# Performance work log

Hardware: AMD Instinct MI355X
Metric: run time of the kernel (lower is better)

## Reference

```python
import jax, jax.numpy as jnp
import numpy as np

D = 1024       # d_model
DR = 1024      # d_rec
FFN = 4096     # ffn_inner
K = 4          # conv_kernel
B, T = 2, 4096
CHUNK = 64
EPS = 1e-6


def setup_inputs() -> dict:
    key = jax.random.key(0)
    ks = jax.random.split(key, 8)
    s = lambda k, shape, scale: jax.random.normal(k, shape, jnp.float32) * scale
    db = np.zeros((DR,), np.float32)
    q = DR // 4
    db[:q] = -2.2
    db[q:3 * q] = 0.0
    db[3 * q:] = 4.6
    return {
        "x": s(ks[0], (B, T, D), 1.0),
        "pre_norm_w": jnp.ones((D,), jnp.float32),
        "conv_w": s(ks[1], (D, 1, K), 0.3),
        "conv_b": jnp.zeros((D,), jnp.float32),
        "w_a": s(ks[2], (DR, D), 0.02),
        "w_i": s(ks[3], (DR, D), 0.02),
        "w_v": s(ks[4], (DR, D), 0.02),
        "out_proj_w": s(ks[5], (D, DR), 0.02),
        "decay_bias": jnp.asarray(db),
        "ffn_norm_w": jnp.ones((D,), jnp.float32),
        "w_gate_up": s(ks[6], (2 * FFN, D), 0.02),
        "w_down": s(ks[7], (D, FFN), 0.02),
    }


def rmsnorm(x, w):
    return x * jax.lax.rsqrt(jnp.mean(x * x, axis=-1, keepdims=True) + EPS) * w


def lin(x, w):  # nn.Linear weight layout (out, in)
    return jnp.einsum('btd,od->bto', x, w)


def causal_conv(h, w, b):
    # depthwise causal conv: h (B,T,D), w (D,1,K)
    hc = jnp.transpose(h, (0, 2, 1))  # (B,D,T)
    out = jax.lax.conv_general_dilated(
        hc, w, window_strides=(1,), padding=[(K - 1, 0)],
        dimension_numbers=('NCH', 'OIH', 'NCH'), feature_group_count=D)
    return jnp.transpose(out, (0, 2, 1)) + b


def chunked_scan(a, v):
    b, s, d = a.shape
    pad = (-s) % CHUNK
    af = jnp.pad(a, ((0, 0), (0, pad), (0, 0)), constant_values=1.0)
    vf = jnp.pad(v, ((0, 0), (0, pad), (0, 0)))
    n = (s + pad) // CHUNK
    dc = af.reshape(b, n, CHUNK, d)
    vc = vf.reshape(b, n, CHUNK, d)
    cum_decay = jnp.exp(jnp.cumsum(jnp.log(jnp.clip(dc, 1e-10)), axis=2))
    intra = cum_decay * jnp.cumsum(vc / jnp.clip(cum_decay, 1e-10), axis=2)

    def step(state, xs):
        cd, it = xs  # (B,CHUNK,d) each
        cs = it + cd * state[:, None, :]
        return cs[:, -1], cs

    _, states = jax.lax.scan(
        step, jnp.zeros((b, d), jnp.float32),
        (jnp.transpose(cum_decay, (1, 0, 2, 3)), jnp.transpose(intra, (1, 0, 2, 3))))
    return jnp.transpose(states, (1, 0, 2, 3)).reshape(b, n * CHUNK, d)[:, :s]


def reference(x, pre_norm_w, conv_w, conv_b, w_a, w_i, w_v, out_proj_w,
              decay_bias, ffn_norm_w, w_gate_up, w_down):
    h = rmsnorm(x, pre_norm_w)
    h = causal_conv(h, conv_w, conv_b)
    a = jax.nn.sigmoid(lin(h, w_a) + decay_bias)
    i_gate = jax.nn.sigmoid(lin(h, w_i))
    v = lin(h, w_v)
    input_signal = jnp.sqrt(jnp.clip(1.0 - a * a, 1e-8)) * (i_gate * v)
    rec_out = chunked_scan(a, input_signal).astype(x.dtype)
    x = x + lin(rec_out, out_proj_w)
    hn = rmsnorm(x, ffn_norm_w)
    gu = lin(hn, w_gate_up)
    gate, up = gu[..., :FFN], gu[..., FFN:]
    x = x + lin(jax.nn.silu(gate) * up, w_down)
    return x
```

## Files before the change

### kernel.cpp

```cpp
#include <hip/hip_runtime.h>

typedef __bf16 bf16_t;
typedef bf16_t bf16x4 __attribute__((ext_vector_type(4)));
typedef bf16_t bf16x8 __attribute__((ext_vector_type(8)));
typedef float f32x4 __attribute__((ext_vector_type(4)));

#define DD 1024
#define TT 4096

__device__ __forceinline__ void gload16(const void* g, void* l) {
    __builtin_amdgcn_global_load_lds(
        (const __attribute__((address_space(1))) void*)g,
        (__attribute__((address_space(3))) void*)l, 16, 0, 0);
}

__global__ __launch_bounds__(256) void cvt_bf16_k(const float* __restrict__ s,
                                                  bf16_t* __restrict__ d, int n) {
    int i = (blockIdx.x * 256 + threadIdx.x) * 4;
    if (i < n) {
        const float4 v = *(const float4*)(s + i);
        bf16x4 o;
        o[0] = (bf16_t)v.x; o[1] = (bf16_t)v.y; o[2] = (bf16_t)v.z; o[3] = (bf16_t)v.w;
        *(bf16x4*)(d + i) = o;
    }
}

__global__ __launch_bounds__(256) void cvt_ileave_k(const float* __restrict__ s0,
                                                    const float* __restrict__ s1,
                                                    bf16_t* __restrict__ d, int total) {
    int i = (blockIdx.x * 256 + threadIdx.x) * 4;
    if (i < total) {
        const int rp = i >> 10, k = i & 1023;
        const int c = rp >> 1;
        const float* src = ((rp & 1) ? s1 : s0) + (long)c * 1024 + k;
        const float4 v = *(const float4*)src;
        bf16x4 o;
        o[0] = (bf16_t)v.x; o[1] = (bf16_t)v.y; o[2] = (bf16_t)v.z; o[3] = (bf16_t)v.w;
        *(bf16x4*)(d + i) = o;
    }
}

__global__ __launch_bounds__(256) void rmsnorm_k(const float* __restrict__ x,
                                                 const float* __restrict__ w,
                                                 bf16_t* __restrict__ ob) {
    const long row = blockIdx.x;
    const float* xr = x + row * DD;
    const int t4 = threadIdx.x * 4;
    float4 v = *(const float4*)(xr + t4);
    float s = v.x*v.x + v.y*v.y + v.z*v.z + v.w*v.w;
    #pragma unroll
    for (int off = 1; off < 64; off <<= 1) s += __shfl_xor(s, off);
    __shared__ float red[4];
    if ((threadIdx.x & 63) == 0) red[threadIdx.x >> 6] = s;
    __syncthreads();
    float tot = red[0] + red[1] + red[2] + red[3];
    float sc = rsqrtf(tot * (1.0f / DD) + 1e-6f);
    float4 wv = *(const float4*)(w + t4);
    bf16x4 o;
    o[0] = (bf16_t)(v.x*sc*wv.x); o[1] = (bf16_t)(v.y*sc*wv.y);
    o[2] = (bf16_t)(v.z*sc*wv.z); o[3] = (bf16_t)(v.w*sc*wv.w);
    *(bf16x4*)(ob + row * DD + t4) = o;
}

__global__ __launch_bounds__(256) void conv_k(const bf16_t* __restrict__ h,
                                              const float* __restrict__ cw,
                                              const float* __restrict__ cb,
                                              bf16_t* __restrict__ hc) {
    const long idx = (long)blockIdx.x * 256 + threadIdx.x;
    const int d = (int)(idx & (DD - 1));
    const long bt = idx >> 10;
    const int t = (int)(bt & (TT - 1));
    const float w0 = cw[d*4+0], w1 = cw[d*4+1], w2 = cw[d*4+2], w3 = cw[d*4+3];
    const bf16_t* hp = h + bt * DD + d;
    float acc = cb[d] + (float)hp[0] * w3;
    if (t >= 1) acc += (float)hp[-DD]     * w2;
    if (t >= 2) acc += (float)hp[-2*DD]   * w1;
    if (t >= 3) acc += (float)hp[-3*DD]   * w0;
    hc[idx] = (bf16_t)acc;
}

__global__ __launch_bounds__(256) void scan1_k(const float* __restrict__ ap,
                                               const bf16_t* __restrict__ sp,
                                               float* __restrict__ cd63,
                                               float* __restrict__ i63) {
    const int d = blockIdx.x * 256 + threadIdx.x;
    const int c = blockIdx.y;
    const int b = blockIdx.z;
    const long rowbase = (long)b * TT + (long)c * 64;
    float la = 0.0f, rs = 0.0f, cdv = 0.0f, it = 0.0f;
    for (int t = 0; t < 64; t++) {
        const long off = (rowbase + t) * DD + d;
        const float a = ap[off];
        const float s = (float)sp[off];
        const float sig = sqrtf(fmaxf(1.0f - a * a, 1e-8f)) * s;
        la += __logf(fmaxf(a, 1e-10f));
        cdv = __expf(la);
        rs += sig / fmaxf(cdv, 1e-10f);
        it = cdv * rs;
    }
    const long o = ((long)b * 64 + c) * DD + d;
    cd63[o] = cdv;
    i63[o]  = it;
}

__global__ __launch_bounds__(256) void scan2_k(const float* __restrict__ cd63,
                                               const float* __restrict__ i63,
                                               float* __restrict__ carry_in) {
    const int g = blockIdx.x * 256 + threadIdx.x;
    const int b = g >> 10, d = g & (DD - 1);
    float st = 0.0f;
    for (int c = 0; c < 64; c++) {
        const long o = ((long)b * 64 + c) * DD + d;
        carry_in[o] = st;
        st = i63[o] + cd63[o] * st;
    }
}

__global__ __launch_bounds__(256) void scan3_k(const float* __restrict__ ap,
                                               const bf16_t* __restrict__ sp,
                                               const float* __restrict__ carry_in,
                                               bf16_t* __restrict__ rec) {
    const int d = blockIdx.x * 256 + threadIdx.x;
    const int c = blockIdx.y;
    const int b = blockIdx.z;
    const long rowbase = (long)b * TT + (long)c * 64;
    const float carry = carry_in[((long)b * 64 + c) * DD + d];
    float la = 0.0f, rs = 0.0f;
    for (int t = 0; t < 64; t++) {
        const long off = (rowbase + t) * DD + d;
        const float a = ap[off];
        const float s = (float)sp[off];
        const float sig = sqrtf(fmaxf(1.0f - a * a, 1e-8f)) * s;
        la += __logf(fmaxf(a, 1e-10f));
        const float cdv = __expf(la);
        rs += sig / fmaxf(cdv, 1e-10f);
        rec[off] = (bf16_t)(cdv * rs + cdv * carry);
    }
}

enum { EPI_AIV = 0, EPI_ADDRES = 1, EPI_GU = 3 };

template<int EPI, int NREP>
__global__ __launch_bounds__(512, 2) void gemm2p_k(const bf16_t* __restrict__ Ag,
                                                   const bf16_t* __restrict__ Bg,
                                                   int M, int N, int K,
                                                   float* outF, bf16_t* outB,
                                                   const float* aux, int ldc) {
    constexpr int BN  = NREP * 64;
    constexpr int ASZ = 16384;
    constexpr int BSZ = BN * 64;
    constexpr int BUF = ASZ + BSZ;
    extern __shared__ bf16_t smem[];
    const int tid = threadIdx.x;
    const int l = tid & 63;
    const int w = tid >> 6;
    const int wm = w >> 2, wn = w & 3;

    const int gx = gridDim.x;
    const int gy = gridDim.y;
    const int lin = blockIdx.y * gx + blockIdx.x;
    long row0, col0;
    if ((gy & 7) == 0) {
        const int rpc = gy >> 3;
        const int q = lin >> 3;
        row0 = (long)((lin & 7) * rpc + q % rpc) * 256;
        col0 = (long)(q / rpc) * (long)BN;
    } else {
        row0 = (long)blockIdx.y * 256;
        col0 = (long)blockIdx.x * BN;
    }

    const int srow = l >> 3;
    const int scol = ((l & 7) ^ srow) * 8;
    const long aBase = row0 + srow;
    const long bBase = col0 + srow;
    const int R0a = w * 32;
    const int R0b = w * (BN / 8);

    const int NT = K >> 6;
    f32x4 acc[8][NREP] = {};

    const int lq2 = (l >> 4) * 16;
    const int rA = wm * 128 + (l & 15);
    const int rB = wn * (NREP * 16) + (l & 15);
    const int eA0 = rA * 64 + ((lq2 ^ ((rA & 7) << 4)) >> 1);
    const int eB0 = ASZ + rB * 64 + ((lq2 ^ ((rB & 7) << 4)) >> 1);

    #define STAGE_A(tt, off)                                                          \
        { const long kgk = (long)(tt) * 64 + scol;                                    \
          _Pragma("unroll")                                                           \
          for (int i = 0; i < 4; i++)                                                 \
              gload16(Ag + (aBase + R0a + i * 8) * (long)K + kgk,                     \
                      &smem[(off) + (R0a + i * 8) * 64]); }
    #define STAGE_B(tt, off)                                                          \
        { const long kgk = (long)(tt) * 64 + scol;                                    \
          _Pragma("unroll")                                                           \
          for (int i = 0; i < NREP; i++)                                              \
              gload16(Bg + (bBase + R0b + i * 8) * (long)K + kgk,                     \
                      &smem[(off) + ASZ + (R0b + i * 8) * 64]); }

    STAGE_A(0, 0); STAGE_B(0, 0);
    STAGE_A(1, BUF); STAGE_B(1, BUF);
    if constexpr (NREP == 4) { asm volatile("s_waitcnt vmcnt(8)" ::: "memory"); }
    else                     { asm volatile("s_waitcnt vmcnt(6)" ::: "memory"); }
    asm volatile("s_barrier" ::: "memory");

    bf16x8 pA[2][4], pB[2][NREP];
    #pragma unroll
    for (int kk = 0; kk < 2; kk++) {
        const int xo = kk * 32;
        #pragma unroll
        for (int n = 0; n < NREP; n++)
            pB[kk][n] = *(const bf16x8*)&smem[(eB0 ^ xo) + n * 1024];
        #pragma unroll
        for (int m = 0; m < 4; m++)
            pA[kk][m] = *(const bf16x8*)&smem[(eA0 ^ xo) + m * 1024];
    }

    for (int t = 0; t < NT; t++) {
        const int co = (t & 1) ? BUF : 0;
        const int oo = BUF - co;
        bf16x8 a1[2][4];

        __builtin_amdgcn_s_setprio(1);
        #pragma unroll
        for (int kk = 0; kk < 2; kk++)
            #pragma unroll
            for (int m = 0; m < 4; m++)
                #pragma unroll
                for (int n = 0; n < NREP; n++)
                    acc[m][n] = __builtin_amdgcn_mfma_f32_16x16x32_bf16(pA[kk][m], pB[kk][n], acc[m][n], 0, 0, 0);
        __builtin_amdgcn_s_setprio(0);
        #pragma unroll
        for (int kk = 0; kk < 2; kk++) {
            const int xo = kk * 32;
            #pragma unroll
            for (int m = 0; m < 4; m++)
                a1[kk][m] = *(const bf16x8*)&smem[co + (eA0 ^ xo) + 4096 + m * 1024];
        }
        asm volatile("s_barrier" ::: "memory");

        if (t + 2 < NT) { STAGE_A(t + 2, co); STAGE_B(t + 2, co); }
        __builtin_amdgcn_s_setprio(1);
        #pragma unroll
        for (int kk = 0; kk < 2; kk++)
            #pragma unroll
            for (int m = 0; m < 4; m++)
                #pragma unroll
                for (int n = 0; n < NREP; n++)
                    acc[m + 4][n] = __builtin_amdgcn_mfma_f32_16x16x32_bf16(a1[kk][m], pB[kk][n], acc[m + 4][n], 0, 0, 0);
        __builtin_amdgcn_s_setprio(0);
        if (t + 2 < NT) {
            if constexpr (NREP == 4) { asm volatile("s_waitcnt vmcnt(8)" ::: "memory"); }
            else                     { asm volatile("s_waitcnt vmcnt(6)" ::: "memory"); }
        } else if (t + 1 < NT) {
            asm volatile("s_waitcnt vmcnt(0)" ::: "memory");
        }
        asm volatile("s_barrier" ::: "memory");
        if (t + 1 < NT) {
            #pragma unroll
            for (int kk = 0; kk < 2; kk++) {
                const int xo = kk * 32;
                #pragma unroll
                for (int n = 0; n < NREP; n++)
                    pB[kk][n] = *(const bf16x8*)&smem[oo + (eB0 ^ xo) + n * 1024];
                #pragma unroll
                for (int m = 0; m < 4; m++)
                    pA[kk][m] = *(const bf16x8*)&smem[oo + (eA0 ^ xo) + m * 1024];
            }
        }
    }
    #undef STAGE_A
    #undef STAGE_B

    #pragma unroll
    for (int m = 0; m < 8; m++) {
        const long r0 = row0 + wm * 128 + m * 16 + (l >> 4) * 4;
        #pragma unroll
        for (int n = 0; n < NREP; n++) {
            const long cc = col0 + wn * (NREP * 16) + n * 16 + (l & 15);
            f32x4 v = acc[m][n];
            #pragma unroll
            for (int j = 0; j < 4; j++) {
                const long r = r0 + j;
                const float xv = v[j];
                if (EPI == EPI_AIV) {
                    if (cc < 1024) {
                        outF[r * ldc + cc] = 1.0f / (1.0f + __expf(-(xv + aux[cc])));
                    } else {
                        const float px = __shfl_xor(xv, 1);
                        if ((l & 1) == 0)
                            outB[r * ldc + ((cc - 1024) >> 1)] =
                                (bf16_t)(px / (1.0f + __expf(-xv)));
                    }
                } else if (EPI == EPI_ADDRES) {
                    outF[r * ldc + cc] = xv + aux[r * ldc + cc];
                } else {
                    const float px = __shfl_xor(xv, 1);
                    if ((l & 1) == 0)
                        outB[r * ldc + (cc >> 1)] = (bf16_t)(xv / (1.0f + __expf(-xv)) * px);
                }
            }
        }
    }
}

extern "C" void kernel_launch(void* const* d_in, const int* in_sizes, int n_in,
                              void* d_out, int out_size, void* d_ws, size_t ws_size,
                              hipStream_t stream) {
    const float* x   = (const float*)d_in[0];
    const float* pnw = (const float*)d_in[1];
    const float* cw  = (const float*)d_in[2];
    const float* cb  = (const float*)d_in[3];
    const float* wa  = (const float*)d_in[4];
    const float* wi  = (const float*)d_in[5];
    const float* wv  = (const float*)d_in[6];
    const float* wop = (const float*)d_in[7];
    const float* db  = (const float*)d_in[8];
    const float* fnw = (const float*)d_in[9];
    const float* wgu = (const float*)d_in[10];
    const float* wdn = (const float*)d_in[11];
    float* out = (float*)d_out;

    char* ws = (char*)d_ws;
    bf16_t* wab   = (bf16_t*)(ws + 0);
    bf16_t* wivb  = (bf16_t*)(ws + 2097152);
    bf16_t* wopb  = (bf16_t*)(ws + 6291456);
    bf16_t* wgub  = (bf16_t*)(ws + 8388608);
    bf16_t* wdnb  = (bf16_t*)(ws + 25165824);
    bf16_t* hb    = (bf16_t*)(ws + 33554432);
    bf16_t* hn    = hb;
    bf16_t* hc    = (bf16_t*)(ws + 50331648);
    bf16_t* rec   = hc;
    float*  a_p   = (float*)(ws + 67108864);
    bf16_t* s_b   = (bf16_t*)(ws + 100663296);
    bf16_t* act   = (bf16_t*)(ws + 67108864);
    float*  cd63  = (float*)(ws + 134217728);
    float*  i63   = (float*)(ws + 134742016);
    float*  carry = (float*)(ws + 135266304);

    const int LDS4 = 131072;
    const int LDS2 = 98304;
    hipFuncSetAttribute((const void*)gemm2p_k<EPI_AIV, 4>,    hipFuncAttributeMaxDynamicSharedMemorySize, LDS4);
    hipFuncSetAttribute((const void*)gemm2p_k<EPI_ADDRES, 2>, hipFuncAttributeMaxDynamicSharedMemorySize, LDS2);
    hipFuncSetAttribute((const void*)gemm2p_k<EPI_GU, 4>,     hipFuncAttributeMaxDynamicSharedMemorySize, LDS4);

    cvt_bf16_k  <<<1024, 256, 0, stream>>>(wa,  wab,  1048576);
    cvt_ileave_k<<<2048, 256, 0, stream>>>(wi,  wv, wivb, 2097152);
    cvt_bf16_k  <<<1024, 256, 0, stream>>>(wop, wopb, 1048576);
    cvt_ileave_k<<<8192, 256, 0, stream>>>(wgu, wgu + 4194304, wgub, 8388608);
    cvt_bf16_k  <<<4096, 256, 0, stream>>>(wdn, wdnb, 4194304);

    rmsnorm_k<<<8192, 256, 0, stream>>>(x, pnw, hb);
    conv_k<<<32768, 256, 0, stream>>>(hb, cw, cb, hc);

    gemm2p_k<EPI_AIV, 4><<<dim3(12, 32), 512, LDS4, stream>>>(hc, wab, 8192, 3072, 1024,
                                                              a_p, s_b, db, 1024);
    scan1_k<<<dim3(4, 64, 2), 256, 0, stream>>>(a_p, s_b, cd63, i63);
    scan2_k<<<8, 256, 0, stream>>>(cd63, i63, carry);
    scan3_k<<<dim3(4, 64, 2), 256, 0, stream>>>(a_p, s_b, carry, rec);

    gemm2p_k<EPI_ADDRES, 2><<<dim3(8, 32), 512, LDS2, stream>>>(rec, wopb, 8192, 1024, 1024,
                                                                out, nullptr, x, 1024);
    rmsnorm_k<<<8192, 256, 0, stream>>>(out, fnw, hn);
    gemm2p_k<EPI_GU, 4><<<dim3(32, 32), 512, LDS4, stream>>>(hn, wgub, 8192, 8192, 1024,
                                                             nullptr, act, nullptr, 4096);
    gemm2p_k<EPI_ADDRES, 2><<<dim3(8, 32), 512, LDS2, stream>>>(act, wdnb, 8192, 1024, 4096,
                                                                out, nullptr, out, 1024);
}
```

Before: 493.8 us.

## Merge weight conversion launches and split fused a/i/v GEMM into two GEMMs

Five weight-conversion kernels become two launches that each cover several tensors, which cuts launch overhead. The fused a/i/v projection GEMM, which branched on column inside its epilogue, is split into a BN=128 sigmoid-bias GEMM for a and a BN=256 GEMM for the interleaved i/v product. The split removes divergent epilogue paths and lets the a GEMM use a smaller tile, but it adds one launch and changes the grid shapes. The two GEMMs now read the activation matrix twice.

Result: faster. 462.3 us (-6.4%).

```diff
diff --git a/kernel.cpp b/kernel.cpp
--- a/kernel.cpp
+++ b/kernel.cpp
@@ -14,30 +14,45 @@
         (__attribute__((address_space(3))) void*)l, 16, 0, 0);
 }
 
-__global__ __launch_bounds__(256) void cvt_bf16_k(const float* __restrict__ s,
-                                                  bf16_t* __restrict__ d, int n) {
-    int i = (blockIdx.x * 256 + threadIdx.x) * 4;
-    if (i < n) {
-        const float4 v = *(const float4*)(s + i);
-        bf16x4 o;
-        o[0] = (bf16_t)v.x; o[1] = (bf16_t)v.y; o[2] = (bf16_t)v.z; o[3] = (bf16_t)v.w;
-        *(bf16x4*)(d + i) = o;
-    }
-}
-
-__global__ __launch_bounds__(256) void cvt_ileave_k(const float* __restrict__ s0,
-                                                    const float* __restrict__ s1,
-                                                    bf16_t* __restrict__ d, int total) {
-    int i = (blockIdx.x * 256 + threadIdx.x) * 4;
-    if (i < total) {
-        const int rp = i >> 10, k = i & 1023;
-        const int c = rp >> 1;
-        const float* src = ((rp & 1) ? s1 : s0) + (long)c * 1024 + k;
-        const float4 v = *(const float4*)src;
-        bf16x4 o;
-        o[0] = (bf16_t)v.x; o[1] = (bf16_t)v.y; o[2] = (bf16_t)v.z; o[3] = (bf16_t)v.w;
-        *(bf16x4*)(d + i) = o;
-    }
+__global__ __launch_bounds__(256) void cvt3_k(const float* __restrict__ s0,
+                                              const float* __restrict__ s1,
+                                              const float* __restrict__ s2,
+                                              bf16_t* __restrict__ d0,
+                                              bf16_t* __restrict__ d1,
+                                              bf16_t* __restrict__ d2) {
+    const int i = (blockIdx.x * 256 + threadIdx.x) * 4;
+    const float* s; bf16_t* d; int off;
+    if (i < 1048576)            { s = s0; d = d0; off = i; }
+    else if (i < 2097152)       { s = s1; d = d1; off = i - 1048576; }
+    else                        { s = s2; d = d2; off = i - 2097152; }
+    const float4 v = *(const float4*)(s + off);
+    bf16x4 o;
+    o[0] = (bf16_t)v.x; o[1] = (bf16_t)v.y; o[2] = (bf16_t)v.z; o[3] = (bf16_t)v.w;
+    *(bf16x4*)(d + off) = o;
+}
+
+__global__ __launch_bounds__(256) void cvt_ilv2_k(const float* __restrict__ wi,
+                                                  const float* __restrict__ wv,
+                                                  bf16_t* __restrict__ wivb,
+                                                  const float* __restrict__ wgu,
+                                                  bf16_t* __restrict__ wgub) {
+    const int i = (blockIdx.x * 256 + threadIdx.x) * 4;
+    const float* src; bf16_t* dst; int idx;
+    if (i < 2097152) {
+        idx = i;
+        const int rp = idx >> 10, k = idx & 1023, c = rp >> 1;
+        src = ((rp & 1) ? wv : wi) + (long)c * 1024 + k;
+        dst = wivb + idx;
+    } else {
+        idx = i - 2097152;
+        const int rp = idx >> 10, k = idx & 1023, c = rp >> 1;
+        src = ((rp & 1) ? (wgu + 4194304) : wgu) + (long)c * 1024 + k;
+        dst = wgub + idx;
+    }
+    const float4 v = *(const float4*)src;
+    bf16x4 o;
+    o[0] = (bf16_t)v.x; o[1] = (bf16_t)v.y; o[2] = (bf16_t)v.z; o[3] = (bf16_t)v.w;
+    *(bf16x4*)dst = o;
 }
 
 __global__ __launch_bounds__(256) void rmsnorm_k(const float* __restrict__ x,
@@ -138,7 +153,7 @@
     }
 }
 
-enum { EPI_AIV = 0, EPI_ADDRES = 1, EPI_GU = 3 };
+enum { EPI_SIGB = 0, EPI_ADDRES = 1, EPI_IV = 2, EPI_GU = 3 };
 
 template<int EPI, int NREP>
 __global__ __launch_bounds__(512, 2) void gemm2p_k(const bf16_t* __restrict__ Ag,
@@ -284,17 +299,14 @@
             for (int j = 0; j < 4; j++) {
                 const long r = r0 + j;
                 const float xv = v[j];
-                if (EPI == EPI_AIV) {
-                    if (cc < 1024) {
-                        outF[r * ldc + cc] = 1.0f / (1.0f + __expf(-(xv + aux[cc])));
-                    } else {
-                        const float px = __shfl_xor(xv, 1);
-                        if ((l & 1) == 0)
-                            outB[r * ldc + ((cc - 1024) >> 1)] =
-                                (bf16_t)(px / (1.0f + __expf(-xv)));
-                    }
+                if (EPI == EPI_SIGB) {
+                    outF[r * ldc + cc] = 1.0f / (1.0f + __expf(-(xv + aux[cc])));
                 } else if (EPI == EPI_ADDRES) {
                     outF[r * ldc + cc] = xv + aux[r * ldc + cc];
+                } else if (EPI == EPI_IV) {
+                    const float px = __shfl_xor(xv, 1);
+                    if ((l & 1) == 0)
+                        outB[r * ldc + (cc >> 1)] = (bf16_t)(px / (1.0f + __expf(-xv)));
                 } else {
                     const float px = __shfl_xor(xv, 1);
                     if ((l & 1) == 0)
@@ -341,21 +353,21 @@
 
     const int LDS4 = 131072;
     const int LDS2 = 98304;
-    hipFuncSetAttribute((const void*)gemm2p_k<EPI_AIV, 4>,    hipFuncAttributeMaxDynamicSharedMemorySize, LDS4);
+    hipFuncSetAttribute((const void*)gemm2p_k<EPI_SIGB, 2>,   hipFuncAttributeMaxDynamicSharedMemorySize, LDS2);
+    hipFuncSetAttribute((const void*)gemm2p_k<EPI_IV, 4>,     hipFuncAttributeMaxDynamicSharedMemorySize, LDS4);
     hipFuncSetAttribute((const void*)gemm2p_k<EPI_ADDRES, 2>, hipFuncAttributeMaxDynamicSharedMemorySize, LDS2);
     hipFuncSetAttribute((const void*)gemm2p_k<EPI_GU, 4>,     hipFuncAttributeMaxDynamicSharedMemorySize, LDS4);
 
-    cvt_bf16_k  <<<1024, 256, 0, stream>>>(wa,  wab,  1048576);
-    cvt_ileave_k<<<2048, 256, 0, stream>>>(wi,  wv, wivb, 2097152);
-    cvt_bf16_k  <<<1024, 256, 0, stream>>>(wop, wopb, 1048576);
-    cvt_ileave_k<<<8192, 256, 0, stream>>>(wgu, wgu + 4194304, wgub, 8388608);
-    cvt_bf16_k  <<<4096, 256, 0, stream>>>(wdn, wdnb, 4194304);
+    cvt3_k    <<<6144, 256, 0, stream>>>(wa, wop, wdn, wab, wopb, wdnb);
+    cvt_ilv2_k<<<10240, 256, 0, stream>>>(wi, wv, wivb, wgu, wgub);
 
     rmsnorm_k<<<8192, 256, 0, stream>>>(x, pnw, hb);
     conv_k<<<32768, 256, 0, stream>>>(hb, cw, cb, hc);
 
-    gemm2p_k<EPI_AIV, 4><<<dim3(12, 32), 512, LDS4, stream>>>(hc, wab, 8192, 3072, 1024,
-                                                              a_p, s_b, db, 1024);
+    gemm2p_k<EPI_SIGB, 2><<<dim3(8, 32), 512, LDS2, stream>>>(hc, wab,  8192, 1024, 1024,
+                                                              a_p, nullptr, db, 1024);
+    gemm2p_k<EPI_IV, 4>  <<<dim3(8, 32), 512, LDS4, stream>>>(hc, wivb, 8192, 2048, 1024,
+                                                              nullptr, s_b, nullptr, 1024);
     scan1_k<<<dim3(4, 64, 2), 256, 0, stream>>>(a_p, s_b, cd63, i63);
     scan2_k<<<8, 256, 0, stream>>>(cd63, i63, carry);
     scan3_k<<<dim3(4, 64, 2), 256, 0, stream>>>(a_p, s_b, carry, rec);
```
